# Kernel optimization log

Hardware: AMD Instinct MI355X
Metric: run time of the kernel (lower is better)

Reference implementation:

```python
import jax, jax.numpy as jnp
import numpy as np

N = 8192
IN_F = 128
OUT_F = 64
ALPHA = 0.2  # LeakyReLU slope
NEG_FILL = -9e15


def setup_inputs() -> dict:
    key = jax.random.key(0)
    k1, k2, k3, k4 = jax.random.split(key, 4)
    inp = jax.random.normal(k1, (N, IN_F), dtype=jnp.float32)
    adj = jax.random.randint(k2, (N, N), 0, 2, dtype=jnp.int32)
    W = jax.random.normal(k3, (IN_F, OUT_F), dtype=jnp.float32) * (1.414 / np.sqrt(IN_F))
    a = jax.random.normal(k4, (2 * OUT_F, 1), dtype=jnp.float32) * 0.1
    return {"input": inp, "adj": adj, "W": W, "a": a}


def reference(input, adj, W, a):
    # h: [N, F]
    h = input @ W
    a1 = a[:OUT_F, 0]   # [F]
    a2 = a[OUT_F:, 0]   # [F]
    # e_ij = leakyrelu(h_i . a1 + h_j . a2)  -- avoids O(N^2 * 2F) concat
    f1 = h @ a1  # [N]
    f2 = h @ a2  # [N]
    e = jax.nn.leaky_relu(f1[:, None] + f2[None, :], negative_slope=ALPHA)  # [N, N]
    scores = jnp.where(adj > 0, e, NEG_FILL)
    attn = jax.nn.softmax(scores, axis=1)  # [N, N]
    h_prime = attn @ h  # [N, F]
    return jax.nn.elu(h_prime)
```

## Files before the change

### kernel.cpp

```cpp
#include <hip/hip_runtime.h>

#define N 8192
#define IN_F 128
#define OUT_F 64
#define ALPHA 0.2f

#define RB 32
#define JT 128
#define TB 512
#define JC 8

typedef int          iv4    __attribute__((ext_vector_type(4)));
typedef unsigned int uv4    __attribute__((ext_vector_type(4)));
typedef unsigned int uv2    __attribute__((ext_vector_type(2)));
typedef __bf16       bf16x8 __attribute__((ext_vector_type(8)));
typedef float        f32x4  __attribute__((ext_vector_type(4)));

__device__ __forceinline__ unsigned short f2bf(float x) {
  unsigned u = __float_as_uint(x);
  u += 0x7fffu + ((u >> 16) & 1u);
  return (unsigned short)(u >> 16);
}
__device__ __forceinline__ float bf2f(unsigned short b) {
  return __uint_as_float(((unsigned)b) << 16);
}

__global__ __launch_bounds__(256) void gat_prep(
    const float* __restrict__ input, const float* __restrict__ W,
    const float* __restrict__ a,
    unsigned short* __restrict__ ht, float* __restrict__ f1,
    float* __restrict__ f2, float* __restrict__ bmax)
{
  __shared__ float Ws[IN_F * OUT_F];
  __shared__ float ins[8][IN_F];
  __shared__ __align__(16) unsigned short Hts[OUT_F][8];
  __shared__ float bm[4];
  int t = threadIdx.x;

  const float4* W4 = (const float4*)W;
  float4* Ws4 = (float4*)Ws;
#pragma unroll
  for (int k = 0; k < 8; ++k) Ws4[t + 256 * k] = W4[t + 256 * k];

  int row0 = blockIdx.x * 8;
  const float4* in4 = (const float4*)(input + (size_t)row0 * IN_F);
  ((float4*)&ins[0][0])[t] = in4[t];
  __syncthreads();

  int w = t >> 6, o = t & 63;
  float a1v = a[o], a2v = a[OUT_F + o];
  float pmax = -3.4e38f;

#pragma unroll
  for (int p = 0; p < 2; ++p) {
    int r = p * 4 + w;
    int i = row0 + r;
    const float4* iv = (const float4*)&ins[r][0];
    float acc = 0.f;
#pragma unroll
    for (int k4 = 0; k4 < 32; ++k4) {
      float4 v = iv[k4];
      acc += v.x * Ws[(k4 * 4 + 0) * OUT_F + o];
      acc += v.y * Ws[(k4 * 4 + 1) * OUT_F + o];
      acc += v.z * Ws[(k4 * 4 + 2) * OUT_F + o];
      acc += v.w * Ws[(k4 * 4 + 3) * OUT_F + o];
    }
    Hts[o][r] = f2bf(acc);
    float p1 = acc * a1v, p2 = acc * a2v;
#pragma unroll
    for (int m = 32; m >= 1; m >>= 1) {
      p1 += __shfl_xor(p1, m, 64);
      p2 += __shfl_xor(p2, m, 64);
    }
    pmax = fmaxf(pmax, p2);
    if (o == 0) {
      f1[i] = p1;
      f2[i] = p2;
    }
  }
  if (o == 0) bm[w] = pmax;
  __syncthreads();
  if (t < 64) {
    uv4 v = *(const uv4*)&Hts[t][0];
    *(uv4*)&ht[(size_t)t * N + row0] = v;
  }
  if (t == 0)
    bmax[blockIdx.x] = fmaxf(fmaxf(bm[0], bm[1]), fmaxf(bm[2], bm[3]));
}

__global__ __launch_bounds__(TB) void gat_part(
    const int* __restrict__ adj, const unsigned short* __restrict__ ht,
    const float* __restrict__ f1, const float* __restrict__ f2,
    const float* __restrict__ bmax,
    float* __restrict__ num, float* __restrict__ den, int jcc)
{
  __shared__ __align__(16) unsigned short HtS[2][OUT_F * JT];
  __shared__ __align__(16) unsigned short PS[2][RB * JT];
  __shared__ float F1s[RB];
  __shared__ float Ms[RB];
  __shared__ float gm[8];

  int t = threadIdx.x;
  int ib = blockIdx.x & 255;
  int jc = blockIdx.x >> 8;
  int i0 = ib * RB;
  int T = (N / JT) / jcc;

  {
    float v = fmaxf(bmax[t], bmax[t + 512]);
#pragma unroll
    for (int m = 32; m >= 1; m >>= 1) v = fmaxf(v, __shfl_xor(v, m, 64));
    if ((t & 63) == 0) gm[t >> 6] = v;
  }
  __syncthreads();
  if (t < RB) {
    float g = gm[0];
#pragma unroll
    for (int k = 1; k < 8; ++k) g = fmaxf(g, gm[k]);
    float f1v = f1[i0 + t];
    F1s[t] = f1v;
    float e = f1v + g;
    Ms[t] = e > 0.f ? e : ALPHA * e;
  }

  int jq = t & 31, rp = t >> 5;
  int so = t >> 3, sc = t & 7;
  int w = t >> 6, l = t & 63;
  int m0 = (w & 1) * 16, n0 = (w >> 1) * 16;
  int arow = m0 + (l & 15);
  int bcol = n0 + (l & 15);
  int kg = (l >> 4) * 16;
  unsigned aswz = (unsigned)((arow & 7) << 4);
  unsigned bswz = (unsigned)((bcol & 7) << 4);
  unsigned sswz = (unsigned)((so & 7) << 4);
  unsigned pswz = (unsigned)((rp & 7) << 4);

  float lsum0 = 0.f, lsum1 = 0.f;
  f32x4 acc = {0.f, 0.f, 0.f, 0.f};

  int jt0 = jc * T, jt1 = (jc + 1) * T;
  const int* arow0 = adj + (size_t)(i0 + rp) * N;
  const int* arow1 = adj + (size_t)(i0 + rp + 16) * N;

  iv4 av0 = __builtin_nontemporal_load((const iv4*)(arow0 + jt0 * JT) + jq);
  iv4 av1 = __builtin_nontemporal_load((const iv4*)(arow1 + jt0 * JT) + jq);
  __syncthreads();

  int buf = 0;
  for (int jt = jt0; jt < jt1; ++jt) {
    int j0 = jt * JT;
    char* HtSb = (char*)&HtS[buf][0];
    char* PSb = (char*)&PS[buf][0];

    {
      const unsigned short* src = ht + (size_t)so * N + j0 + sc * 8;
      uv4 h0 = *(const uv4*)(src);
      uv4 h1 = *(const uv4*)(src + 64);
      *(uv4*)(HtSb + (((unsigned)(so * 256 + sc * 16)) ^ sswz)) = h0;
      *(uv4*)(HtSb + (((unsigned)(so * 256 + 128 + sc * 16)) ^ sswz)) = h1;
    }

    {
      float4 fv = *(const float4*)(f2 + j0 + jq * 4);
      float e; float4 pv; uv2 w2;

      float f1v = F1s[rp], mv = Ms[rp];
      e = f1v + fv.x; e = e > 0.f ? e : ALPHA * e; pv.x = (av0.x > 0) ? __expf(e - mv) : 0.f;
      e = f1v + fv.y; e = e > 0.f ? e : ALPHA * e; pv.y = (av0.y > 0) ? __expf(e - mv) : 0.f;
      e = f1v + fv.z; e = e > 0.f ? e : ALPHA * e; pv.z = (av0.z > 0) ? __expf(e - mv) : 0.f;
      e = f1v + fv.w; e = e > 0.f ? e : ALPHA * e; pv.w = (av0.w > 0) ? __expf(e - mv) : 0.f;
      unsigned short b0 = f2bf(pv.x), b1 = f2bf(pv.y), b2 = f2bf(pv.z), b3 = f2bf(pv.w);
      lsum0 += (bf2f(b0) + bf2f(b1)) + (bf2f(b2) + bf2f(b3));
      w2.x = (unsigned)b0 | ((unsigned)b1 << 16);
      w2.y = (unsigned)b2 | ((unsigned)b3 << 16);
      *(uv2*)(PSb + (((unsigned)(rp * 256 + jq * 8)) ^ pswz)) = w2;

      f1v = F1s[rp + 16]; mv = Ms[rp + 16];
      e = f1v + fv.x; e = e > 0.f ? e : ALPHA * e; pv.x = (av1.x > 0) ? __expf(e - mv) : 0.f;
      e = f1v + fv.y; e = e > 0.f ? e : ALPHA * e; pv.y = (av1.y > 0) ? __expf(e - mv) : 0.f;
      e = f1v + fv.z; e = e > 0.f ? e : ALPHA * e; pv.z = (av1.z > 0) ? __expf(e - mv) : 0.f;
      e = f1v + fv.w; e = e > 0.f ? e : ALPHA * e; pv.w = (av1.w > 0) ? __expf(e - mv) : 0.f;
      b0 = f2bf(pv.x); b1 = f2bf(pv.y); b2 = f2bf(pv.z); b3 = f2bf(pv.w);
      lsum1 += (bf2f(b0) + bf2f(b1)) + (bf2f(b2) + bf2f(b3));
      w2.x = (unsigned)b0 | ((unsigned)b1 << 16);
      w2.y = (unsigned)b2 | ((unsigned)b3 << 16);
      *(uv2*)(PSb + (((unsigned)((rp + 16) * 256 + jq * 8)) ^ pswz)) = w2;
    }

    if (jt + 1 < jt1) {
      av0 = __builtin_nontemporal_load((const iv4*)(arow0 + (jt + 1) * JT) + jq);
      av1 = __builtin_nontemporal_load((const iv4*)(arow1 + (jt + 1) * JT) + jq);
    }
    __syncthreads();

#pragma unroll
    for (int ks = 0; ks < 4; ++ks) {
      bf16x8 a8 = __builtin_bit_cast(bf16x8,
          *(const uv4*)(PSb + (((unsigned)(arow * 256 + ks * 64 + kg)) ^ aswz)));
      bf16x8 b8 = __builtin_bit_cast(bf16x8,
          *(const uv4*)(HtSb + (((unsigned)(bcol * 256 + ks * 64 + kg)) ^ bswz)));
      acc = __builtin_amdgcn_mfma_f32_16x16x32_bf16(a8, b8, acc, 0, 0, 0);
    }
    buf ^= 1;
  }

#pragma unroll
  for (int m = 16; m >= 1; m >>= 1) {
    lsum0 += __shfl_xor(lsum0, m, 64);
    lsum1 += __shfl_xor(lsum1, m, 64);
  }
  if ((t & 31) == 0) {
    den[(size_t)jc * N + i0 + rp] = lsum0;
    den[(size_t)jc * N + i0 + rp + 16] = lsum1;
  }

  int crow = i0 + m0 + ((l >> 4) << 2);
  float* np = num + ((size_t)jc * N + crow) * OUT_F + n0 + (l & 15);
  np[0 * OUT_F] = acc[0];
  np[1 * OUT_F] = acc[1];
  np[2 * OUT_F] = acc[2];
  np[3 * OUT_F] = acc[3];
}

__global__ __launch_bounds__(256) void gat_reduce(
    const unsigned short* __restrict__ ht, const float* __restrict__ num,
    const float* __restrict__ den, float* __restrict__ out, int jcc)
{
  int t = threadIdx.x;
  int i = blockIdx.x * 16 + (t >> 4);
  int o4 = t & 15;

  float d = 0.f;
  for (int c = 0; c < jcc; ++c) d += den[(size_t)c * N + i];

  float a0 = 0.f, a1 = 0.f, a2 = 0.f, a3 = 0.f;
  for (int c = 0; c < jcc; ++c) {
    float4 v = *(const float4*)&num[(((size_t)c * N) + i) * OUT_F + o4 * 4];
    a0 += v.x; a1 += v.y; a2 += v.z; a3 += v.w;
  }

  if (d <= 0.f) {
    a0 = a1 = a2 = a3 = 0.f;
    for (int j = 0; j < N; ++j) {
      a0 += bf2f(ht[(size_t)(o4 * 4 + 0) * N + j]);
      a1 += bf2f(ht[(size_t)(o4 * 4 + 1) * N + j]);
      a2 += bf2f(ht[(size_t)(o4 * 4 + 2) * N + j]);
      a3 += bf2f(ht[(size_t)(o4 * 4 + 3) * N + j]);
    }
    d = (float)N;
  }
  float inv = 1.f / d;
  a0 *= inv; a1 *= inv; a2 *= inv; a3 *= inv;
  float4 r4;
  r4.x = a0 > 0.f ? a0 : expm1f(a0);
  r4.y = a1 > 0.f ? a1 : expm1f(a1);
  r4.z = a2 > 0.f ? a2 : expm1f(a2);
  r4.w = a3 > 0.f ? a3 : expm1f(a3);
  *(float4*)&out[(size_t)i * OUT_F + o4 * 4] = r4;
}

extern "C" void kernel_launch(void* const* d_in, const int* in_sizes, int n_in,
                              void* d_out, int out_size, void* d_ws, size_t ws_size,
                              hipStream_t stream) {
  const float* input = (const float*)d_in[0];
  const int*   adj   = (const int*)d_in[1];
  const float* W     = (const float*)d_in[2];
  const float* a     = (const float*)d_in[3];
  float* out = (float*)d_out;

  unsigned short* ht = (unsigned short*)d_ws;
  float* f1 = (float*)(ht + (size_t)N * OUT_F);
  float* f2 = f1 + N;
  float* bmax = f2 + N;
  float* den = bmax + N / 8;
  float* num = den + (size_t)JC * N;
  size_t need = (size_t)((char*)(num + (size_t)JC * N * OUT_F) - (char*)d_ws);

  int jcc = (ws_size >= need) ? JC : 1;

  gat_prep<<<N / 8, 256, 0, stream>>>(input, W, a, ht, f1, f2, bmax);
  gat_part<<<jcc * (N / RB), TB, 0, stream>>>(adj, ht, f1, f2, bmax, num, den, jcc);
  gat_reduce<<<N / 16, 256, 0, stream>>>(ht, num, den, out, jcc);
}
```

Baseline: 84.71 us.

## Compute attention probabilities directly in MFMA A-operand registers with 128-row blocks

Restructures the partial aggregation kernel so each wave owns 16 rows and computes the masked exp probabilities straight into the bf16 A-operand layout of the MFMA, dropping the shared-memory P buffer and its extra barrier traffic. Each block now covers 128 rows, so every h tile staged in LDS is reused across four times as many rows, and each wave issues four MFMAs per k-step across all 64 output columns. The grid shrinks to 512 blocks and more accumulators and adjacency loads are held per thread, which raises register pressure and reduces the number of blocks available to hide latency.

```diff
diff --git a/kernel.cpp b/kernel.cpp
--- a/kernel.cpp
+++ b/kernel.cpp
@@ -5,14 +5,13 @@
 #define OUT_F 64
 #define ALPHA 0.2f
 
-#define RB 32
+#define RBK 128
 #define JT 128
 #define TB 512
 #define JC 8
 
 typedef int          iv4    __attribute__((ext_vector_type(4)));
 typedef unsigned int uv4    __attribute__((ext_vector_type(4)));
-typedef unsigned int uv2    __attribute__((ext_vector_type(2)));
 typedef __bf16       bf16x8 __attribute__((ext_vector_type(8)));
 typedef float        f32x4  __attribute__((ext_vector_type(4)));
 
@@ -88,22 +87,19 @@
     bmax[blockIdx.x] = fmaxf(fmaxf(bm[0], bm[1]), fmaxf(bm[2], bm[3]));
 }
 
-__global__ __launch_bounds__(TB) void gat_part(
+__global__ __launch_bounds__(TB, 4) void gat_part(
     const int* __restrict__ adj, const unsigned short* __restrict__ ht,
     const float* __restrict__ f1, const float* __restrict__ f2,
     const float* __restrict__ bmax,
     float* __restrict__ num, float* __restrict__ den, int jcc)
 {
   __shared__ __align__(16) unsigned short HtS[2][OUT_F * JT];
-  __shared__ __align__(16) unsigned short PS[2][RB * JT];
-  __shared__ float F1s[RB];
-  __shared__ float Ms[RB];
   __shared__ float gm[8];
 
   int t = threadIdx.x;
-  int ib = blockIdx.x & 255;
-  int jc = blockIdx.x >> 8;
-  int i0 = ib * RB;
+  int ib = blockIdx.x & 63;
+  int jc = blockIdx.x >> 6;
+  int i0 = ib * RBK;
   int T = (N / JT) / jcc;
 
   {
@@ -113,44 +109,81 @@
     if ((t & 63) == 0) gm[t >> 6] = v;
   }
   __syncthreads();
-  if (t < RB) {
-    float g = gm[0];
-#pragma unroll
-    for (int k = 1; k < 8; ++k) g = fmaxf(g, gm[k]);
-    float f1v = f1[i0 + t];
-    F1s[t] = f1v;
-    float e = f1v + g;
-    Ms[t] = e > 0.f ? e : ALPHA * e;
-  }
-
-  int jq = t & 31, rp = t >> 5;
+  float g = gm[0];
+#pragma unroll
+  for (int k = 1; k < 8; ++k) g = fmaxf(g, gm[k]);
+
+  int w = t >> 6, l = t & 63;
+  int kq = l >> 4;
+  int i = i0 + w * 16 + (l & 15);
+  float f1v = f1[i];
+  float e0 = f1v + g;
+  float mv = e0 > 0.f ? e0 : ALPHA * e0;
+
   int so = t >> 3, sc = t & 7;
-  int w = t >> 6, l = t & 63;
-  int m0 = (w & 1) * 16, n0 = (w >> 1) * 16;
-  int arow = m0 + (l & 15);
-  int bcol = n0 + (l & 15);
-  int kg = (l >> 4) * 16;
-  unsigned aswz = (unsigned)((arow & 7) << 4);
-  unsigned bswz = (unsigned)((bcol & 7) << 4);
   unsigned sswz = (unsigned)((so & 7) << 4);
-  unsigned pswz = (unsigned)((rp & 7) << 4);
-
-  float lsum0 = 0.f, lsum1 = 0.f;
-  f32x4 acc = {0.f, 0.f, 0.f, 0.f};
+
+  int kg = kq * 16;
+  unsigned bswz = (unsigned)((l & 7) << 4);
+
+  float lsum = 0.f;
+  f32x4 acc0 = {0.f,0.f,0.f,0.f}, acc1 = {0.f,0.f,0.f,0.f};
+  f32x4 acc2 = {0.f,0.f,0.f,0.f}, acc3 = {0.f,0.f,0.f,0.f};
 
   int jt0 = jc * T, jt1 = (jc + 1) * T;
-  const int* arow0 = adj + (size_t)(i0 + rp) * N;
-  const int* arow1 = adj + (size_t)(i0 + rp + 16) * N;
-
-  iv4 av0 = __builtin_nontemporal_load((const iv4*)(arow0 + jt0 * JT) + jq);
-  iv4 av1 = __builtin_nontemporal_load((const iv4*)(arow1 + jt0 * JT) + jq);
-  __syncthreads();
+  const int* ar = adj + (size_t)i * N + kq * 8;
+
+  iv4 a0l = __builtin_nontemporal_load((const iv4*)(ar + jt0 * JT + 0));
+  iv4 a0h = __builtin_nontemporal_load((const iv4*)(ar + jt0 * JT + 0) + 1);
+  iv4 a1l = __builtin_nontemporal_load((const iv4*)(ar + jt0 * JT + 32));
+  iv4 a1h = __builtin_nontemporal_load((const iv4*)(ar + jt0 * JT + 32) + 1);
+  iv4 a2l = __builtin_nontemporal_load((const iv4*)(ar + jt0 * JT + 64));
+  iv4 a2h = __builtin_nontemporal_load((const iv4*)(ar + jt0 * JT + 64) + 1);
+  iv4 a3l = __builtin_nontemporal_load((const iv4*)(ar + jt0 * JT + 96));
+  iv4 a3h = __builtin_nontemporal_load((const iv4*)(ar + jt0 * JT + 96) + 1);
 
   int buf = 0;
+
+#define KS_BODY(KS, AVL, AVH)                                                 \
+  {                                                                           \
+    float4 fv0 = *(const float4*)(f2 + j0 + (KS) * 32 + kq * 8);              \
+    float4 fv1 = *(const float4*)(f2 + j0 + (KS) * 32 + kq * 8 + 4);          \
+    float e; unsigned short c0,c1,c2,c3,c4,c5,c6,c7;                          \
+    e = f1v + fv0.x; e = e > 0.f ? e : ALPHA * e; c0 = (AVL.x > 0) ? f2bf(__expf(e - mv)) : 0; \
+    e = f1v + fv0.y; e = e > 0.f ? e : ALPHA * e; c1 = (AVL.y > 0) ? f2bf(__expf(e - mv)) : 0; \
+    e = f1v + fv0.z; e = e > 0.f ? e : ALPHA * e; c2 = (AVL.z > 0) ? f2bf(__expf(e - mv)) : 0; \
+    e = f1v + fv0.w; e = e > 0.f ? e : ALPHA * e; c3 = (AVL.w > 0) ? f2bf(__expf(e - mv)) : 0; \
+    e = f1v + fv1.x; e = e > 0.f ? e : ALPHA * e; c4 = (AVH.x > 0) ? f2bf(__expf(e - mv)) : 0; \
+    e = f1v + fv1.y; e = e > 0.f ? e : ALPHA * e; c5 = (AVH.y > 0) ? f2bf(__expf(e - mv)) : 0; \
+    e = f1v + fv1.z; e = e > 0.f ? e : ALPHA * e; c6 = (AVH.z > 0) ? f2bf(__expf(e - mv)) : 0; \
+    e = f1v + fv1.w; e = e > 0.f ? e : ALPHA * e; c7 = (AVH.w > 0) ? f2bf(__expf(e - mv)) : 0; \
+    lsum += ((bf2f(c0)+bf2f(c1)) + (bf2f(c2)+bf2f(c3)))                       \
+          + ((bf2f(c4)+bf2f(c5)) + (bf2f(c6)+bf2f(c7)));                      \
+    uv4 w4;                                                                   \
+    w4.x = (unsigned)c0 | ((unsigned)c1 << 16);                               \
+    w4.y = (unsigned)c2 | ((unsigned)c3 << 16);                               \
+    w4.z = (unsigned)c4 | ((unsigned)c5 << 16);                               \
+    w4.w = (unsigned)c6 | ((unsigned)c7 << 16);                               \
+        \
+    if (jt + 1 < jt1) {                                                       \
+      AVL = __builtin_nontemporal_load((const iv4*)(ar + (jt + 1) * JT + (KS) * 32)); \
+      AVH = __builtin_nontemporal_load((const iv4*)(ar + (jt + 1) * JT + (KS) * 32) + 1); \
+    }                                                                         \
+    bf16x8 a8 = __builtin_bit_cast(bf16x8, w4);                               \
+    bf16x8 b8;                                                                \
+    b8 = __builtin_bit_cast(bf16x8, *(const uv4*)(HtSb + (((unsigned)((0 * 16 + (l & 15)) * 256 + (KS) * 64 + kg)) ^ bswz))); \
+    acc0 = __builtin_amdgcn_mfma_f32_16x16x32_bf16(a8, b8, acc0, 0, 0, 0);    \
+    b8 = __builtin_bit_cast(bf16x8, *(const uv4*)(HtSb + (((unsigned)((1 * 16 + (l & 15)) * 256 + (KS) * 64 + kg)) ^ bswz))); \
+    acc1 = __builtin_amdgcn_mfma_f32_16x16x32_bf16(a8, b8, acc1, 0, 0, 0);    \
+    b8 = __builtin_bit_cast(bf16x8, *(const uv4*)(HtSb + (((unsigned)((2 * 16 + (l & 15)) * 256 + (KS) * 64 + kg)) ^ bswz))); \
+    acc2 = __builtin_amdgcn_mfma_f32_16x16x32_bf16(a8, b8, acc2, 0, 0, 0);    \
+    b8 = __builtin_bit_cast(bf16x8, *(const uv4*)(HtSb + (((unsigned)((3 * 16 + (l & 15)) * 256 + (KS) * 64 + kg)) ^ bswz))); \
+    acc3 = __builtin_amdgcn_mfma_f32_16x16x32_bf16(a8, b8, acc3, 0, 0, 0);    \
+  }
+
   for (int jt = jt0; jt < jt1; ++jt) {
     int j0 = jt * JT;
     char* HtSb = (char*)&HtS[buf][0];
-    char* PSb = (char*)&PS[buf][0];
 
     {
       const unsigned short* src = ht + (size_t)so * N + j0 + sc * 8;
@@ -159,67 +192,33 @@
       *(uv4*)(HtSb + (((unsigned)(so * 256 + sc * 16)) ^ sswz)) = h0;
       *(uv4*)(HtSb + (((unsigned)(so * 256 + 128 + sc * 16)) ^ sswz)) = h1;
     }
-
-    {
-      float4 fv = *(const float4*)(f2 + j0 + jq * 4);
-      float e; float4 pv; uv2 w2;
-
-      float f1v = F1s[rp], mv = Ms[rp];
-      e = f1v + fv.x; e = e > 0.f ? e : ALPHA * e; pv.x = (av0.x > 0) ? __expf(e - mv) : 0.f;
-      e = f1v + fv.y; e = e > 0.f ? e : ALPHA * e; pv.y = (av0.y > 0) ? __expf(e - mv) : 0.f;
-      e = f1v + fv.z; e = e > 0.f ? e : ALPHA * e; pv.z = (av0.z > 0) ? __expf(e - mv) : 0.f;
-      e = f1v + fv.w; e = e > 0.f ? e : ALPHA * e; pv.w = (av0.w > 0) ? __expf(e - mv) : 0.f;
-      unsigned short b0 = f2bf(pv.x), b1 = f2bf(pv.y), b2 = f2bf(pv.z), b3 = f2bf(pv.w);
-      lsum0 += (bf2f(b0) + bf2f(b1)) + (bf2f(b2) + bf2f(b3));
-      w2.x = (unsigned)b0 | ((unsigned)b1 << 16);
-      w2.y = (unsigned)b2 | ((unsigned)b3 << 16);
-      *(uv2*)(PSb + (((unsigned)(rp * 256 + jq * 8)) ^ pswz)) = w2;
-
-      f1v = F1s[rp + 16]; mv = Ms[rp + 16];
-      e = f1v + fv.x; e = e > 0.f ? e : ALPHA * e; pv.x = (av1.x > 0) ? __expf(e - mv) : 0.f;
-      e = f1v + fv.y; e = e > 0.f ? e : ALPHA * e; pv.y = (av1.y > 0) ? __expf(e - mv) : 0.f;
-      e = f1v + fv.z; e = e > 0.f ? e : ALPHA * e; pv.z = (av1.z > 0) ? __expf(e - mv) : 0.f;
-      e = f1v + fv.w; e = e > 0.f ? e : ALPHA * e; pv.w = (av1.w > 0) ? __expf(e - mv) : 0.f;
-      b0 = f2bf(pv.x); b1 = f2bf(pv.y); b2 = f2bf(pv.z); b3 = f2bf(pv.w);
-      lsum1 += (bf2f(b0) + bf2f(b1)) + (bf2f(b2) + bf2f(b3));
-      w2.x = (unsigned)b0 | ((unsigned)b1 << 16);
-      w2.y = (unsigned)b2 | ((unsigned)b3 << 16);
-      *(uv2*)(PSb + (((unsigned)((rp + 16) * 256 + jq * 8)) ^ pswz)) = w2;
-    }
-
-    if (jt + 1 < jt1) {
-      av0 = __builtin_nontemporal_load((const iv4*)(arow0 + (jt + 1) * JT) + jq);
-      av1 = __builtin_nontemporal_load((const iv4*)(arow1 + (jt + 1) * JT) + jq);
-    }
     __syncthreads();
 
-#pragma unroll
-    for (int ks = 0; ks < 4; ++ks) {
-      bf16x8 a8 = __builtin_bit_cast(bf16x8,
-          *(const uv4*)(PSb + (((unsigned)(arow * 256 + ks * 64 + kg)) ^ aswz)));
-      bf16x8 b8 = __builtin_bit_cast(bf16x8,
-          *(const uv4*)(HtSb + (((unsigned)(bcol * 256 + ks * 64 + kg)) ^ bswz)));
-      acc = __builtin_amdgcn_mfma_f32_16x16x32_bf16(a8, b8, acc, 0, 0, 0);
-    }
+    KS_BODY(0, a0l, a0h)
+    KS_BODY(1, a1l, a1h)
+    KS_BODY(2, a2l, a2h)
+    KS_BODY(3, a3l, a3h)
+
     buf ^= 1;
   }
-
-#pragma unroll
-  for (int m = 16; m >= 1; m >>= 1) {
-    lsum0 += __shfl_xor(lsum0, m, 64);
-    lsum1 += __shfl_xor(lsum1, m, 64);
-  }
-  if ((t & 31) == 0) {
-    den[(size_t)jc * N + i0 + rp] = lsum0;
-    den[(size_t)jc * N + i0 + rp + 16] = lsum1;
-  }
-
-  int crow = i0 + m0 + ((l >> 4) << 2);
-  float* np = num + ((size_t)jc * N + crow) * OUT_F + n0 + (l & 15);
-  np[0 * OUT_F] = acc[0];
-  np[1 * OUT_F] = acc[1];
-  np[2 * OUT_F] = acc[2];
-  np[3 * OUT_F] = acc[3];
+#undef KS_BODY
+
+  lsum += __shfl_xor(lsum, 16, 64);
+  lsum += __shfl_xor(lsum, 32, 64);
+  if (l < 16)
+    den[(size_t)jc * N + i] = lsum;
+
+  {
+    int crow = i0 + w * 16 + (kq << 2);
+    float* np = num + ((size_t)jc * N + crow) * OUT_F + (l & 15);
+#pragma unroll
+    for (int rg = 0; rg < 4; ++rg) {
+      np[(size_t)rg * OUT_F + 0]  = acc0[rg];
+      np[(size_t)rg * OUT_F + 16] = acc1[rg];
+      np[(size_t)rg * OUT_F + 32] = acc2[rg];
+      np[(size_t)rg * OUT_F + 48] = acc3[rg];
+    }
+  }
 }
 
 __global__ __launch_bounds__(256) void gat_reduce(
@@ -279,6 +278,6 @@
   int jcc = (ws_size >= need) ? JC : 1;
 
   gat_prep<<<N / 8, 256, 0, stream>>>(input, W, a, ht, f1, f2, bmax);
-  gat_part<<<jcc * (N / RB), TB, 0, stream>>>(adj, ht, f1, f2, bmax, num, den, jcc);
+  gat_part<<<jcc * (N / RBK), TB, 0, stream>>>(adj, ht, f1, f2, bmax, num, den, jcc);
   gat_reduce<<<N / 16, 256, 0, stream>>>(ht, num, den, out, jcc);
 }
```

New measurement: 115.0 us. 35.7% more time.
